# Kernel optimization log

Hardware: AMD Instinct MI355X
Metric: run time of the kernel (lower is better)

Reference implementation:

```python
import jax, jax.numpy as jnp
import numpy as np

T, X_D, M_N, CHUNK, REDUCE = 2048, 2048, 64, 64, 8
M_D = X_D // REDUCE          # 256
DECAY_D = M_D // 4           # 64
H_D = X_D * 2                # factor=2
FF_D = 256 * round(int(H_D * (2.0 / 3.0)) / 256)  # 2816


def setup_inputs() -> dict:
    key = jax.random.key(0)
    ks = jax.random.split(key, 20)
    def lin(k, out_d, in_d):
        return (jax.random.normal(k, (out_d, in_d), jnp.float32) / np.sqrt(in_d).astype(np.float32))
    return {
        "xs": jax.random.normal(ks[0], (T, X_D), jnp.float32),
        "attn_q": lin(ks[1], X_D // REDUCE, X_D),
        "attn_k": lin(ks[2], X_D // REDUCE, X_D // REDUCE),
        "attn_v": lin(ks[3], X_D, X_D),
        "attn_o": lin(ks[4], X_D, X_D),
        "attn_r": lin(ks[5], X_D, X_D),
        "mem_f": lin(ks[6], M_N, X_D),
        "mem_q": lin(ks[7], M_D, X_D),
        "mem_k": lin(ks[8], M_D, M_D),
        "mem_v": lin(ks[9], M_D, X_D),
        "mem_o": lin(ks[10], X_D, M_D),
        "mem_r": lin(ks[11], X_D, X_D),
        "mem_beta": -jnp.ones((M_N, M_D), jnp.float32),
        "mem_decay": 3.0 * jnp.ones((M_N, DECAY_D), jnp.float32),
        "mem_l": jax.random.uniform(ks[12], (M_N, M_D), dtype=jnp.float32),
        "ff_in1": lin(ks[13], FF_D, X_D),
        "ff_in2": lin(ks[14], FF_D, X_D),
        "ff_out": lin(ks[15], X_D, FF_D),
        "sn1_g": jnp.sqrt(jnp.float32(X_D)),
        "sn2_g": jnp.sqrt(jnp.float32(X_D)),
    }


def _rotate_half(x):
    x1 = x[..., ::2]
    x2 = x[..., 1::2]
    return jnp.stack((-x2, x1), axis=-1).reshape(x.shape)


def _scale_norm(x, g):
    return x * (g / (jnp.linalg.norm(x, axis=-1, keepdims=True) + 1e-8))


def _attn(xs, Wq, Wk, Wv, Wo, Wr):
    n = CHUNK
    q = xs @ Wq.T                       # (T, dk)
    k = q @ Wk.T                        # k is computed from q (as in source)
    v = xs @ Wv.T                       # (T, x_d)
    c = xs.shape[0] // n
    dk = q.shape[-1]
    q = q.reshape(c, n, dk)
    k = k.reshape(c, n, dk)
    v = v.reshape(c, n, v.shape[-1])

    def with_prev(a):                   # prepend previous chunk (zero for chunk 0)
        prev = jnp.concatenate([jnp.zeros_like(a[:1]), a[:-1]], axis=0)
        return jnp.concatenate([prev, a], axis=1)   # (c, 2n, d)

    k2, v2 = with_prev(k), with_prev(v)

    # RoPE over 2n key positions; queries take the last n positions
    inv_freq = 1.0 / (10000.0 ** (jnp.arange(0, dk, 2, dtype=jnp.float32) / dk))
    ang = jnp.arange(2 * n, dtype=jnp.float32)[:, None] * inv_freq[None, :]
    sin = jnp.repeat(jnp.sin(ang), 2, axis=-1)      # (2n, dk) interleaved
    cos = jnp.repeat(jnp.cos(ang), 2, axis=-1)
    q = q * cos[None, n:] + _rotate_half(q) * sin[None, n:]
    k2 = k2 * cos[None] + _rotate_half(k2) * sin[None]

    qk = jnp.einsum('cnk,cmk->cnm', q, k2) / jnp.sqrt(jnp.float32(dk))
    allowed = jnp.arange(2 * n)[None, :] <= (jnp.arange(n)[:, None] + n)  # tril offset n
    A = jax.nn.softmax(jnp.where(allowed[None], qk, -jnp.inf), axis=-1)
    y = jnp.einsum('cnm,cmv->cnv', A, v2).reshape(xs.shape[0], -1)
    return (y @ Wo.T) * jax.nn.sigmoid(xs @ Wr.T)


def _mem(xs, Wf, Wq, Wk, Wv, Wo, Wr, beta_p, decay_p, l_p):
    v = xs @ Wv.T                                       # (T, m_d)
    f = jax.nn.sigmoid(xs @ Wf.T)[:, :, None]           # (T, m_n, 1)
    beta = jax.nn.sigmoid(beta_p)[None]                 # (1, m_n, m_d)
    gamma = jnp.concatenate(
        [jnp.ones((M_N, M_D - DECAY_D), xs.dtype), jax.nn.sigmoid(decay_p)], axis=1
    )[None]                                             # (1, m_n, m_d)
    ws = (1.0 - f * beta) * gamma                       # (T, m_n, m_d)
    fvs = f * v[:, None, :]                             # (T, m_n, m_d)

    def bin_assoc(ei, ej):
        ai, bi = ei
        aj, bj = ej
        return (aj * ai, aj * bi + bj)

    _, mems = jax.lax.associative_scan(bin_assoc, (ws, fvs), axis=0)  # (T, m_n, m_d)

    q = xs @ Wq.T                                       # (T, m_d)
    k = jnp.einsum('nmd,kd->nmk', mems, Wk) + l_p[None]
    A = jax.nn.softmax(jnp.einsum('nmk,nk->nm', k, q) / jnp.sqrt(jnp.float32(M_D)), axis=-1)
    y = jnp.einsum('nm,nmd->nd', A, mems)
    return (y @ Wo.T) * jax.nn.sigmoid(xs @ Wr.T)


def _ff(xs, W1, W2, Wo):
    return (jax.nn.silu(xs @ W1.T) * (xs @ W2.T)) @ Wo.T


def reference(xs, attn_q, attn_k, attn_v, attn_o, attn_r,
              mem_f, mem_q, mem_k, mem_v, mem_o, mem_r,
              mem_beta, mem_decay, mem_l,
              ff_in1, ff_in2, ff_out, sn1_g, sn2_g):
    xn = _scale_norm(xs, sn1_g)
    xs = (_attn(xn, attn_q, attn_k, attn_v, attn_o, attn_r)
          + _mem(xn, mem_f, mem_q, mem_k, mem_v, mem_o, mem_r, mem_beta, mem_decay, mem_l)
          + xs)
    xs = _ff(_scale_norm(xs, sn2_g), ff_in1, ff_in2, ff_out) + xs
    return xs
```

## Files before the change

kernel.cpp:

```cpp
#include <hip/hip_runtime.h>
#include <math.h>


typedef short bhalf8 __attribute__((ext_vector_type(8)));
typedef float f32x4 __attribute__((ext_vector_type(4)));

#define CC_LD 7168
#define COL_V   0
#define COL_B1  2048
#define COL_B2  4096
#define COL_QB  6144
#define COL_VM  6400
#define COL_QM  6656
#define COL_FG  6912

#define AS1 __attribute__((address_space(1)))
#define AS3 __attribute__((address_space(3)))

__device__ __forceinline__ float sigmoidf_(float x){ return 1.0f/(1.0f+expf(-x)); }

__device__ __forceinline__ unsigned short f2b(float f){
  unsigned u = __float_as_uint(f);
  unsigned r = (u + 0x7fffu + ((u>>16)&1u)) >> 16;
  return (unsigned short)r;
}
__device__ __forceinline__ float b2f(unsigned short h){
  return __uint_as_float(((unsigned)h)<<16);
}

__global__ void k_f2b_all(
    const float* __restrict__ av, const float* __restrict__ ar, const float* __restrict__ mr,
    const float* __restrict__ aq, const float* __restrict__ mv, const float* __restrict__ mq,
    const float* __restrict__ mf, const float* __restrict__ ao, const float* __restrict__ mo,
    const float* __restrict__ f1, const float* __restrict__ f2, const float* __restrict__ fo,
    const float* __restrict__ ak,
    unsigned short* __restrict__ WCAT, unsigned short* __restrict__ AOB,
    unsigned short* __restrict__ MOB, unsigned short* __restrict__ FFW,
    unsigned short* __restrict__ FFOB, unsigned short* __restrict__ AKB){
  int i = blockIdx.x*256 + threadIdx.x;
  const float* s; unsigned short* d; int off;
  if (i < 3571712){
    d = WCAT + (size_t)i*4;
    if      (i < 1048576){ s = av; off = i; }
    else if (i < 2097152){ s = ar; off = i-1048576; }
    else if (i < 3145728){ s = mr; off = i-2097152; }
    else if (i < 3276800){ s = aq; off = i-3145728; }
    else if (i < 3407872){ s = mv; off = i-3276800; }
    else if (i < 3538944){ s = mq; off = i-3407872; }
    else                 { s = mf; off = i-3538944; }
  }
  else if (i < 4620288){ off = i-3571712; s = ao; d = AOB  + (size_t)off*4; }
  else if (i < 4751360){ off = i-4620288; s = mo; d = MOB  + (size_t)off*4; }
  else if (i < 6193152){ off = i-4751360; s = f1;
    int row = off >> 9, c4 = off & 511;
    d = FFW + ((size_t)row*2)*2048 + c4*4; }
  else if (i < 7634944){ off = i-6193152; s = f2;
    int row = off >> 9, c4 = off & 511;
    d = FFW + ((size_t)row*2 + 1)*2048 + c4*4; }
  else if (i < 9076736){ off = i-7634944; s = fo; d = FFOB + (size_t)off*4; }
  else if (i < 9093120){ off = i-9076736; s = ak; d = AKB  + (size_t)off*4; }
  else return;
  float4 v = ((const float4*)s)[off];
  ushort4 o;
  o.x = f2b(v.x); o.y = f2b(v.y); o.z = f2b(v.z); o.w = f2b(v.w);
  *(ushort4*)d = o;
}

__global__ void k_f2bT(const float* __restrict__ s, unsigned short* __restrict__ d){
  int i = blockIdx.x, j = threadIdx.x;
  d[(size_t)j*256 + i] = f2b(s[(size_t)i*256 + j]);
}

__global__ void k_trig(float2* __restrict__ TR){
  int idx = blockIdx.x*256 + threadIdx.x;
  int pos = idx >> 7, j = idx & 127;
  float inv = powf(10000.f, -(float)j/128.f);
  float a = (float)pos * inv;
  TR[idx] = make_float2(cosf(a), sinf(a));
}

__global__ __launch_bounds__(256) void k_scalenorm_b(const float* __restrict__ x,
    const float* __restrict__ g, unsigned short* __restrict__ ob){
  int row = blockIdx.x, tid = threadIdx.x;
  const float* xr = x + (size_t)row*2048;
  float ss = 0.f;
  for (int j = tid; j < 2048; j += 256){ float v = xr[j]; ss += v*v; }
  __shared__ float red[256];
  red[tid] = ss; __syncthreads();
  for (int s = 128; s > 0; s >>= 1){ if (tid < s) red[tid] += red[tid+s]; __syncthreads(); }
  float scale = g[0] / (sqrtf(red[0]) + 1e-8f);
  unsigned short* orow = ob + (size_t)row*2048;
  for (int j4 = tid; j4 < 512; j4 += 256){
    float4 v = *(const float4*)(xr + j4*4);
    ushort4 o;
    o.x = f2b(v.x*scale); o.y = f2b(v.y*scale); o.z = f2b(v.z*scale); o.w = f2b(v.w*scale);
    ((ushort4*)orow)[j4] = o;
  }
}

__global__ __launch_bounds__(256) void k_gemm_p(
    const unsigned short* __restrict__ A, int lda,
    const unsigned short* __restrict__ B,
    float* __restrict__ C, unsigned short* __restrict__ Cb,
    int N, int K, int ldc, int epi,
    const float* __restrict__ add,
    const unsigned short* __restrict__ gate, int gate_ld,
    const unsigned short* A2, const unsigned short* B2, float* C2){
  __shared__ unsigned short LDSu[24576];
  int tid = threadIdx.x;
  int w = tid >> 6, l = tid & 63;
  int bi = blockIdx.y, bj = blockIdx.x;
  const unsigned short* Ap = A; const unsigned short* Bp = B; float* Cp = C;
  if (blockIdx.z){ Ap = A2; Bp = B2; Cp = C2; }
  int m0 = bi*128, n0 = bj*128;
  int wr = w >> 1, wc = w & 1;

  f32x4 acc[4][4];
#pragma unroll
  for (int i=0;i<4;++i)
#pragma unroll
    for (int j=0;j<4;++j){ f32x4 z = {0.f,0.f,0.f,0.f}; acc[i][j] = z; }

  const int r0 = tid >> 2;
  const int gsrc8 = (((tid&3) ^ ((tid>>3)&3)) * 8);

  auto stage = [&](int bs, int kt){
    unsigned short* db = LDSu + bs*8192;
    const unsigned short* ap0 = Ap + (size_t)(m0 + r0)*lda      + kt*32 + gsrc8;
    const unsigned short* ap1 = Ap + (size_t)(m0 + 64 + r0)*lda + kt*32 + gsrc8;
    const unsigned short* bp0 = Bp + (size_t)(n0 + r0)*K        + kt*32 + gsrc8;
    const unsigned short* bp1 = Bp + (size_t)(n0 + 64 + r0)*K   + kt*32 + gsrc8;
    __builtin_amdgcn_global_load_lds((const AS1 void*)ap0, (AS3 void*)(db + tid*8),        16, 0, 0);
    __builtin_amdgcn_global_load_lds((const AS1 void*)ap1, (AS3 void*)(db + 2048 + tid*8), 16, 0, 0);
    __builtin_amdgcn_global_load_lds((const AS1 void*)bp0, (AS3 void*)(db + 4096 + tid*8), 16, 0, 0);
    __builtin_amdgcn_global_load_lds((const AS1 void*)bp1, (AS3 void*)(db + 6144 + tid*8), 16, 0, 0);
  };

  const int nt = K >> 5;
  stage(0, 0);
  stage(1, 1);
  asm volatile("s_waitcnt vmcnt(4)" ::: "memory");
  __builtin_amdgcn_s_barrier();

  const int lr = l & 15;
  const int gsw = (((l>>4) ^ ((l>>1)&3)) * 8);
  const int aoff = (wr*64 + lr)*32 + gsw;
  const int boff = 4096 + (wc*64 + lr)*32 + gsw;

  int cur = 0;
  for (int t = 0; t < nt; ++t){
    if (t + 2 < nt) stage((t+2)%3, t+2);
    const unsigned short* Tb = LDSu + cur*8192;
    bhalf8 af[4], bfr[4];
#pragma unroll
    for (int m=0;m<4;++m) af[m]  = *(const bhalf8*)(Tb + aoff + m*512);
#pragma unroll
    for (int n=0;n<4;++n) bfr[n] = *(const bhalf8*)(Tb + boff + n*512);
    __builtin_amdgcn_s_setprio(1);
#pragma unroll
    for (int m=0;m<4;++m)
#pragma unroll
      for (int n=0;n<4;++n)
        acc[m][n] = __builtin_amdgcn_mfma_f32_16x16x32_bf16(af[m], bfr[n], acc[m][n], 0, 0, 0);
    __builtin_amdgcn_s_setprio(0);
    if (t + 1 < nt){
      if (t + 2 < nt){ asm volatile("s_waitcnt vmcnt(4)" ::: "memory"); }
      else           { asm volatile("s_waitcnt vmcnt(0)" ::: "memory"); }
      __builtin_amdgcn_s_barrier();
      cur = (cur == 2) ? 0 : cur + 1;
    }
  }

#pragma unroll
  for (int m=0;m<4;++m){
    int rowb = m0 + wr*64 + m*16 + ((l>>4)<<2);
#pragma unroll
    for (int r=0;r<4;++r){
      int row = rowb + r;
      size_t rbase = (size_t)row*ldc;
      size_t gbase = (size_t)row*gate_ld;
#pragma unroll
      for (int n=0;n<4;++n){
        int col = n0 + wc*64 + n*16 + (l&15);
        float v = acc[m][n][r];
        if (epi == 4){
          float o = __shfl_xor(v, 1);
          if ((l & 1) == 0)
            Cb[gbase + (col>>1)] = f2b(v*sigmoidf_(v)*o);
          continue;
        }
        if (add) v += add[rbase + col];
        if (epi == 2) v *= sigmoidf_(b2f(gate[gbase + col]));
        if (epi == 3) Cb[rbase + col] = f2b(v);
        else          Cp[rbase + col] = v;
      }
    }
  }
}

__global__ __launch_bounds__(256) void k_gemm_fuse2(
    const unsigned short* __restrict__ A,  const unsigned short* __restrict__ B,
    const unsigned short* __restrict__ A2, const unsigned short* __restrict__ B2,
    const unsigned short* __restrict__ gate1, const unsigned short* __restrict__ gate2,
    const float* __restrict__ xs, float* __restrict__ XS2){
  __shared__ unsigned short LDSu[24576];
  int tid = threadIdx.x;
  int w = tid >> 6, l = tid & 63;
  int bi = blockIdx.y, bj = blockIdx.x;
  int m0 = bi*128, n0 = bj*128;
  int wr = w >> 1, wc = w & 1;

  f32x4 acc[4][4], acc2[4][4];
#pragma unroll
  for (int i=0;i<4;++i)
#pragma unroll
    for (int j=0;j<4;++j){ f32x4 z = {0.f,0.f,0.f,0.f}; acc[i][j] = z; acc2[i][j] = z; }

  const int r0 = tid >> 2;
  const int gsrc8 = (((tid&3) ^ ((tid>>3)&3)) * 8);

  auto stage = [&](int bs, int kt, const unsigned short* Ap, int lda,
                   const unsigned short* Bp, int ldb){
    unsigned short* db = LDSu + bs*8192;
    const unsigned short* ap0 = Ap + (size_t)(m0 + r0)*lda      + kt*32 + gsrc8;
    const unsigned short* ap1 = Ap + (size_t)(m0 + 64 + r0)*lda + kt*32 + gsrc8;
    const unsigned short* bp0 = Bp + (size_t)(n0 + r0)*ldb      + kt*32 + gsrc8;
    const unsigned short* bp1 = Bp + (size_t)(n0 + 64 + r0)*ldb + kt*32 + gsrc8;
    __builtin_amdgcn_global_load_lds((const AS1 void*)ap0, (AS3 void*)(db + tid*8),        16, 0, 0);
    __builtin_amdgcn_global_load_lds((const AS1 void*)ap1, (AS3 void*)(db + 2048 + tid*8), 16, 0, 0);
    __builtin_amdgcn_global_load_lds((const AS1 void*)bp0, (AS3 void*)(db + 4096 + tid*8), 16, 0, 0);
    __builtin_amdgcn_global_load_lds((const AS1 void*)bp1, (AS3 void*)(db + 6144 + tid*8), 16, 0, 0);
  };

  const int lr = l & 15;
  const int gsw = (((l>>4) ^ ((l>>1)&3)) * 8);
  const int aoff = (wr*64 + lr)*32 + gsw;
  const int boff = 4096 + (wc*64 + lr)*32 + gsw;

  {
    const int nt = 64;
    stage(0, 0, A, 2048, B, 2048);
    stage(1, 1, A, 2048, B, 2048);
    asm volatile("s_waitcnt vmcnt(4)" ::: "memory");
    __builtin_amdgcn_s_barrier();
    int cur = 0;
    for (int t = 0; t < nt; ++t){
      if (t + 2 < nt) stage((t+2)%3, t+2, A, 2048, B, 2048);
      const unsigned short* Tb = LDSu + cur*8192;
      bhalf8 af[4], bfr[4];
#pragma unroll
      for (int m=0;m<4;++m) af[m]  = *(const bhalf8*)(Tb + aoff + m*512);
#pragma unroll
      for (int n=0;n<4;++n) bfr[n] = *(const bhalf8*)(Tb + boff + n*512);
      __builtin_amdgcn_s_setprio(1);
#pragma unroll
      for (int m=0;m<4;++m)
#pragma unroll
        for (int n=0;n<4;++n)
          acc[m][n] = __builtin_amdgcn_mfma_f32_16x16x32_bf16(af[m], bfr[n], acc[m][n], 0, 0, 0);
      __builtin_amdgcn_s_setprio(0);
      if (t + 1 < nt){
        if (t + 2 < nt){ asm volatile("s_waitcnt vmcnt(4)" ::: "memory"); }
        else           { asm volatile("s_waitcnt vmcnt(0)" ::: "memory"); }
        __builtin_amdgcn_s_barrier();
        cur = (cur == 2) ? 0 : cur + 1;
      }
    }
  }
  __syncthreads();

  {
    const int nt = 8;
    stage(0, 0, A2, 256, B2, 256);
    stage(1, 1, A2, 256, B2, 256);
    asm volatile("s_waitcnt vmcnt(4)" ::: "memory");
    __builtin_amdgcn_s_barrier();
    int cur = 0;
    for (int t = 0; t < nt; ++t){
      if (t + 2 < nt) stage((t+2)%3, t+2, A2, 256, B2, 256);
      const unsigned short* Tb = LDSu + cur*8192;
      bhalf8 af[4], bfr[4];
#pragma unroll
      for (int m=0;m<4;++m) af[m]  = *(const bhalf8*)(Tb + aoff + m*512);
#pragma unroll
      for (int n=0;n<4;++n) bfr[n] = *(const bhalf8*)(Tb + boff + n*512);
      __builtin_amdgcn_s_setprio(1);
#pragma unroll
      for (int m=0;m<4;++m)
#pragma unroll
        for (int n=0;n<4;++n)
          acc2[m][n] = __builtin_amdgcn_mfma_f32_16x16x32_bf16(af[m], bfr[n], acc2[m][n], 0, 0, 0);
      __builtin_amdgcn_s_setprio(0);
      if (t + 1 < nt){
        if (t + 2 < nt){ asm volatile("s_waitcnt vmcnt(4)" ::: "memory"); }
        else           { asm volatile("s_waitcnt vmcnt(0)" ::: "memory"); }
        __builtin_amdgcn_s_barrier();
        cur = (cur == 2) ? 0 : cur + 1;
      }
    }
  }

#pragma unroll
  for (int m=0;m<4;++m){
    int rowb = m0 + wr*64 + m*16 + ((l>>4)<<2);
#pragma unroll
    for (int r=0;r<4;++r){
      int row = rowb + r;
      size_t gb = (size_t)row*CC_LD;
      size_t rb = (size_t)row*2048;
#pragma unroll
      for (int n=0;n<4;++n){
        int col = n0 + wc*64 + n*16 + (l&15);
        float v = acc[m][n][r]*sigmoidf_(b2f(gate1[gb + col]))
                + acc2[m][n][r]*sigmoidf_(b2f(gate2[gb + col]))
                + xs[rb + col];
        XS2[rb + col] = v;
      }
    }
  }
}

__global__ __launch_bounds__(256) void k_attn_scores_mfma(
    const unsigned short* __restrict__ CCqb, const float* __restrict__ K0,
    const float2* __restrict__ TR, unsigned short* __restrict__ P){
  __shared__ unsigned short Ks[128*256];
  int c = blockIdx.x, tid = threadIdx.x;
  for (int it = 0; it < 16; ++it){
    int id = tid + it*256;
    int m = id >> 5;
    int cs = (id & 31) * 8;
    float v[8];
    if (c == 0 && m < 64){
#pragma unroll
      for (int u=0;u<8;++u) v[u] = 0.f;
    } else {
      int gr = (c-1)*64 + m;
      const float* kr = K0 + (size_t)gr*256 + cs;
      float4 x0 = *(const float4*)kr, x1 = *(const float4*)(kr+4);
      v[0]=x0.x; v[1]=x0.y; v[2]=x0.z; v[3]=x0.w;
      v[4]=x1.x; v[5]=x1.y; v[6]=x1.z; v[7]=x1.w;
#pragma unroll
      for (int p2=0;p2<4;++p2){
        float2 t = TR[m*128 + (cs>>1) + p2];
        float e = v[2*p2], o = v[2*p2+1];
        v[2*p2]   = e*t.x - o*t.y;
        v[2*p2+1] = o*t.x + e*t.y;
      }
    }
    unsigned short pk[8];
#pragma unroll
    for (int u=0;u<8;++u) pk[u] = f2b(v[u]);
    int byte = m*512 + ((cs*2) ^ ((m&7)<<4));
    *(bhalf8*)((char*)&Ks[0] + byte) = *(const bhalf8*)pk;
  }
  __syncthreads();

  int w = tid >> 6, l = tid & 63;
  int lr = l & 15, lkg = l >> 4;
  f32x4 acc[8];
#pragma unroll
  for (int n=0;n<8;++n){ f32x4 z = {0.f,0.f,0.f,0.f}; acc[n] = z; }

  int iq = w*16 + lr;
  const unsigned short* qbase = CCqb + (size_t)(c*64 + iq)*CC_LD;
  int pos = 64 + iq;

  for (int kt = 0; kt < 8; ++kt){
    int k0c = kt*32 + lkg*8;
    bhalf8 q8 = *(const bhalf8*)(qbase + k0c);
    float v[8];
#pragma unroll
    for (int u=0;u<8;++u) v[u] = b2f((unsigned short)(((short*)&q8)[u]));
#pragma unroll
    for (int p2=0;p2<4;++p2){
      float2 t = TR[pos*128 + (k0c>>1) + p2];
      float e = v[2*p2], o = v[2*p2+1];
      v[2*p2]   = e*t.x - o*t.y;
      v[2*p2+1] = o*t.x + e*t.y;
    }
    unsigned short pk[8];
#pragma unroll
    for (int u=0;u<8;++u) pk[u] = f2b(v[u]);
    bhalf8 af = *(const bhalf8*)pk;
#pragma unroll
    for (int n=0;n<8;++n){
      int m = n*16 + lr;
      int byte = m*512 + ((k0c*2) ^ ((m&7)<<4));
      bhalf8 bf = *(const bhalf8*)((const char*)&Ks[0] + byte);
      acc[n] = __builtin_amdgcn_mfma_f32_16x16x32_bf16(af, bf, acc[n], 0, 0, 0);
    }
  }

  int i0 = w*16 + lkg*4;
  float mx[4] = {-1e30f,-1e30f,-1e30f,-1e30f};
  float sm[4] = {0.f,0.f,0.f,0.f};
#pragma unroll
  for (int n=0;n<8;++n){
    int col = n*16 + lr;
#pragma unroll
    for (int r=0;r<4;++r){
      float vv = acc[n][r] * (1.f/16.f);
      if (col > i0 + r + 64) vv = -1e30f;
      acc[n][r] = vv;
      mx[r] = fmaxf(mx[r], vv);
    }
  }
#pragma unroll
  for (int s=1; s<16; s<<=1)
#pragma unroll
    for (int r=0;r<4;++r) mx[r] = fmaxf(mx[r], __shfl_xor(mx[r], s));
#pragma unroll
  for (int n=0;n<8;++n)
#pragma unroll
    for (int r=0;r<4;++r){
      float e = expf(acc[n][r] - mx[r]);
      acc[n][r] = e; sm[r] += e;
    }
#pragma unroll
  for (int s=1; s<16; s<<=1)
#pragma unroll
    for (int r=0;r<4;++r) sm[r] += __shfl_xor(sm[r], s);
  float rcp[4];
#pragma unroll
  for (int r=0;r<4;++r) rcp[r] = 1.f/sm[r];

  unsigned short* Pr = P + (size_t)c*8192;
#pragma unroll
  for (int n=0;n<8;++n){
    int col = n*16 + lr;
#pragma unroll
    for (int r=0;r<4;++r)
      Pr[(i0+r)*128 + col] = f2b(acc[n][r]*rcp[r]);
  }
}

__global__ __launch_bounds__(256) void k_attn_pv_mfma(
    const unsigned short* __restrict__ P, const unsigned short* __restrict__ Vb, int vld,
    unsigned short* __restrict__ Y){
  __shared__ unsigned short Vt[128*128];
  int ct = blockIdx.x, c = blockIdx.y, tid = threadIdx.x;
  {
    int k = tid >> 1;
    int ch = (tid & 1) * 64;
    if (c == 0 && k < 64){
      for (int u=0; u<64; ++u){
        int col = ch + u;
        int byte = col*256 + ((k*2) ^ ((col&7)<<4));
        *(unsigned short*)((char*)&Vt[0] + byte) = 0;
      }
    } else {
      int gr = (c-1)*64 + k;
      const unsigned short* vr = Vb + (size_t)gr*vld + ct*128 + ch;
      for (int u8=0; u8<8; ++u8){
        bhalf8 x = *(const bhalf8*)(vr + u8*8);
#pragma unroll
        for (int u=0;u<8;++u){
          int col = ch + u8*8 + u;
          int byte = col*256 + ((k*2) ^ ((col&7)<<4));
          *(unsigned short*)((char*)&Vt[0] + byte) = (unsigned short)(((short*)&x)[u]);
        }
      }
    }
  }
  __syncthreads();
  int w = tid >> 6, l = tid & 63, lr = l & 15, lkg = l >> 4;
  f32x4 acc[8];
#pragma unroll
  for (int n=0;n<8;++n){ f32x4 z = {0.f,0.f,0.f,0.f}; acc[n] = z; }
  const unsigned short* Pr = P + (size_t)c*8192;
  for (int kt=0; kt<4; ++kt){
    int kb = kt*32 + lkg*8;
    bhalf8 af = *(const bhalf8*)(Pr + (w*16 + lr)*128 + kb);
#pragma unroll
    for (int n=0;n<8;++n){
      int col = n*16 + lr;
      int byte = col*256 + ((kb*2) ^ ((col&7)<<4));
      bhalf8 bf = *(const bhalf8*)((const char*)&Vt[0] + byte);
      acc[n] = __builtin_amdgcn_mfma_f32_16x16x32_bf16(af, bf, acc[n], 0, 0, 0);
    }
  }
  int row0 = c*64 + w*16 + lkg*4;
#pragma unroll
  for (int n=0;n<8;++n){
    int col = ct*128 + n*16 + lr;
#pragma unroll
    for (int r=0;r<4;++r)
      Y[(size_t)(row0+r)*2048 + col] = f2b(acc[n][r]);
  }
}

__global__ __launch_bounds__(256) void k_scan1(const unsigned short* __restrict__ CC,
    const float* __restrict__ beta_p, const float* __restrict__ decay_p,
    float* __restrict__ CP, float* __restrict__ CQ){
  int c = blockIdx.x, mg = blockIdx.y, d = threadIdx.x;
  __shared__ float Fs[512];
  for (int v = threadIdx.x; v < 512; v += 256){
    int s = v >> 3, j = v & 7;
    Fs[v] = sigmoidf_(b2f(CC[(size_t)(c*64+s)*CC_LD + COL_FG + mg*8 + j]));
  }
  __syncthreads();
  float beta[8], gamma[8], Pa[8], Qa[8];
#pragma unroll
  for (int j=0;j<8;++j){
    int m = mg*8+j;
    beta[j]  = sigmoidf_(beta_p[m*256+d]);
    gamma[j] = (d < 192) ? 1.f : sigmoidf_(decay_p[m*64 + (d-192)]);
    Pa[j] = 1.f; Qa[j] = 0.f;
  }
  for (int s = 0; s < 64; ++s){
    float vm = b2f(CC[(size_t)(c*64+s)*CC_LD + COL_VM + d]);
#pragma unroll
    for (int j=0;j<8;++j){
      float f = Fs[s*8+j];
      float w = (1.f - f*beta[j])*gamma[j];
      Pa[j] *= w;
      Qa[j] = w*Qa[j] + f*vm;
    }
  }
#pragma unroll
  for (int j=0;j<8;++j){
    size_t idx = ((size_t)c*64 + mg*8 + j)*256 + d;
    CP[idx] = Pa[j]; CQ[idx] = Qa[j];
  }
}

__global__ __launch_bounds__(256) void k_scan2(const float* __restrict__ CP,
    const float* __restrict__ CQ, float* __restrict__ SIN){
  int m = blockIdx.x, d = threadIdx.x;
  float S = 0.f;
  for (int c = 0; c < 32; ++c){
    size_t idx = ((size_t)c*64 + m)*256 + d;
    SIN[idx] = S;
    S = CP[idx]*S + CQ[idx];
  }
}

__global__ __launch_bounds__(256) void k_scan3(const unsigned short* __restrict__ CC,
    const float* __restrict__ beta_p, const float* __restrict__ decay_p,
    const float* __restrict__ SIN, unsigned short* __restrict__ MEMS){
  int c = blockIdx.x, mg = blockIdx.y, d = threadIdx.x;
  __shared__ float Fs[512];
  for (int v = threadIdx.x; v < 512; v += 256){
    int s = v >> 3, j = v & 7;
    Fs[v] = sigmoidf_(b2f(CC[(size_t)(c*64+s)*CC_LD + COL_FG + mg*8 + j]));
  }
  __syncthreads();
  float beta[8], gamma[8], S[8];
#pragma unroll
  for (int j=0;j<8;++j){
    int m = mg*8+j;
    beta[j]  = sigmoidf_(beta_p[m*256+d]);
    gamma[j] = (d < 192) ? 1.f : sigmoidf_(decay_p[m*64 + (d-192)]);
    S[j] = SIN[((size_t)c*64 + m)*256 + d];
  }
  for (int s = 0; s < 64; ++s){
    float vm = b2f(CC[(size_t)(c*64+s)*CC_LD + COL_VM + d]);
    size_t tb = (size_t)(c*64+s)*64;
#pragma unroll
    for (int j=0;j<8;++j){
      float f = Fs[s*8+j];
      float w = (1.f - f*beta[j])*gamma[j];
      S[j] = w*S[j] + f*vm;
      MEMS[(tb + mg*8 + j)*256 + d] = f2b(S[j]);
    }
  }
}

__global__ __launch_bounds__(256) void k_memread(const unsigned short* __restrict__ MEMS,
    const float* __restrict__ QH, const unsigned short* __restrict__ QMs, int qm_ld,
    const float* __restrict__ L, unsigned short* __restrict__ YMb){
  int t = blockIdx.x, tid = threadIdx.x;
  int wave = tid >> 6, lane = tid & 63;
  __shared__ float anorm[64];
  const unsigned short* Mt = MEMS + (size_t)t*16384;
  float4 qh4 = *(const float4*)(QH + (size_t)t*256 + lane*4);
  ushort4 qmu = *(const ushort4*)(QMs + (size_t)t*qm_ld + lane*4);
  float qm0 = b2f(qmu.x), qm1 = b2f(qmu.y), qm2 = b2f(qmu.z), qm3 = b2f(qmu.w);
  for (int mi = 0; mi < 16; ++mi){
    int m = wave*16 + mi;
    ushort4 su = *(const ushort4*)(Mt + m*256 + lane*4);
    float4 l4 = *(const float4*)(L + (size_t)m*256 + lane*4);
    float p = b2f(su.x)*qh4.x + b2f(su.y)*qh4.y + b2f(su.z)*qh4.z + b2f(su.w)*qh4.w
            + l4.x*qm0 + l4.y*qm1 + l4.z*qm2 + l4.w*qm3;
#pragma unroll
    for (int off = 32; off > 0; off >>= 1) p += __shfl_down(p, off);
    if (lane == 0) anorm[m] = p * (1.f/16.f);
  }
  __syncthreads();
  if (tid < 64){
    float v = anorm[tid];
    float mx = v;
#pragma unroll
    for (int off = 32; off > 0; off >>= 1) mx = fmaxf(mx, __shfl_xor(mx, off));
    float e = expf(v - mx);
    float s = e;
#pragma unroll
    for (int off = 32; off > 0; off >>= 1) s += __shfl_xor(s, off);
    anorm[tid] = e / s;
  }
  __syncthreads();
  float acc = 0.f;
  for (int m = 0; m < 64; ++m) acc += anorm[m]*b2f(Mt[m*256 + tid]);
  YMb[(size_t)t*256 + tid] = f2b(acc);
}

extern "C" void kernel_launch(void* const* d_in, const int* in_sizes, int n_in,
                              void* d_out, int out_size, void* d_ws, size_t ws_size,
                              hipStream_t stream){
  const float* xs        = (const float*)d_in[0];
  const float* attn_q    = (const float*)d_in[1];
  const float* attn_k    = (const float*)d_in[2];
  const float* attn_v    = (const float*)d_in[3];
  const float* attn_o    = (const float*)d_in[4];
  const float* attn_r    = (const float*)d_in[5];
  const float* mem_f     = (const float*)d_in[6];
  const float* mem_q     = (const float*)d_in[7];
  const float* mem_k     = (const float*)d_in[8];
  const float* mem_v     = (const float*)d_in[9];
  const float* mem_o     = (const float*)d_in[10];
  const float* mem_r     = (const float*)d_in[11];
  const float* mem_beta  = (const float*)d_in[12];
  const float* mem_decay = (const float*)d_in[13];
  const float* mem_l     = (const float*)d_in[14];
  const float* ff1       = (const float*)d_in[15];
  const float* ff2       = (const float*)d_in[16];
  const float* ffo       = (const float*)d_in[17];
  const float* sn1       = (const float*)d_in[18];
  const float* sn2       = (const float*)d_in[19];
  float* out = (float*)d_out;
  float* W = (float*)d_ws;

  unsigned short* XNb  = (unsigned short*)(W + 0);
  unsigned short* WCAT = (unsigned short*)(W + 2097152);
  unsigned short* CCb  = (unsigned short*)(W + 9437184);
  unsigned short* AOB  = (unsigned short*)(W + 16777216);
  unsigned short* MOB  = (unsigned short*)(W + 18874368);
  unsigned short* FFW  = (unsigned short*)(W + 19136512);
  unsigned short* FFOB = (unsigned short*)(W + 24903680);
  unsigned short* AKB  = (unsigned short*)(W + 27787264);
  unsigned short* MKTB = (unsigned short*)(W + 27820032);
  unsigned short* Ybb  = (unsigned short*)(W + 27852800);
  float*          XS2  = W + 34144256;
  unsigned short* MEMSb= (unsigned short*)(W + 38338560);
  float*          CP   = W + 55115776;
  float*          CQ   = W + 55640064;
  float*          SIN  = W + 56164352;
  float2*         TRIG = (float2*)(W + 0);
  float*          K0   = W + 32768;
  unsigned short* P    = (unsigned short*)(W + 557056);
  float*          QH   = W + 688128;
  unsigned short* YMb  = (unsigned short*)(W + 1212416);
  unsigned short* XN2b = MEMSb;
  unsigned short* H1b  = (unsigned short*)(W + 40435712);

  dim3 blk(256);

  k_f2b_all<<<dim3(35520), blk, 0, stream>>>(attn_v, attn_r, mem_r, attn_q, mem_v, mem_q,
      mem_f, attn_o, mem_o, ff1, ff2, ffo, attn_k, WCAT, AOB, MOB, FFW, FFOB, AKB);
  k_f2bT<<<dim3(256), blk, 0, stream>>>(mem_k, MKTB);

  k_scalenorm_b<<<dim3(2048), blk, 0, stream>>>(xs, sn1, XNb);

  k_gemm_p<<<dim3(56, 16), blk, 0, stream>>>(XNb, 2048, WCAT, nullptr, CCb, CC_LD, 2048, CC_LD, 3,
      nullptr, nullptr, 0, nullptr, nullptr, nullptr);

  k_trig<<<dim3(64), blk, 0, stream>>>(TRIG);

  k_gemm_p<<<dim3(2, 16, 2), blk, 0, stream>>>(CCb + COL_QB, CC_LD, AKB, K0, nullptr, 256, 256, 256, 0,
      nullptr, nullptr, 0, CCb + COL_QM, MKTB, QH);

  k_attn_scores_mfma<<<dim3(32), blk, 0, stream>>>(CCb + COL_QB, K0, TRIG, P);
  k_attn_pv_mfma<<<dim3(16, 32), blk, 0, stream>>>(P, CCb + COL_V, CC_LD, Ybb);

  k_scan1<<<dim3(32, 8), blk, 0, stream>>>(CCb, mem_beta, mem_decay, CP, CQ);
  k_scan2<<<dim3(64), blk, 0, stream>>>(CP, CQ, SIN);
  k_scan3<<<dim3(32, 8), blk, 0, stream>>>(CCb, mem_beta, mem_decay, SIN, MEMSb);
  k_memread<<<dim3(2048), blk, 0, stream>>>(MEMSb, QH, CCb + COL_QM, CC_LD, mem_l, YMb);

  k_gemm_fuse2<<<dim3(16, 16), blk, 0, stream>>>(Ybb, AOB, YMb, MOB,
      CCb + COL_B1, CCb + COL_B2, xs, XS2);

  k_scalenorm_b<<<dim3(2048), blk, 0, stream>>>(XS2, sn2, XN2b);

  k_gemm_p<<<dim3(44, 16), blk, 0, stream>>>(XN2b, 2048, FFW, nullptr, H1b, 5632, 2048, 5632, 4,
      nullptr, nullptr, 2816, nullptr, nullptr, nullptr);
  k_gemm_p<<<dim3(16, 16), blk, 0, stream>>>(H1b, 2816, FFOB, out, nullptr, 2048, 2816, 2048, 0,
      XS2, nullptr, 0, nullptr, nullptr, nullptr);
}
```

Before: 416.5 us.

## Use 256x256-tile 512-thread GEMM kernel for the two largest projections

Adds a new GEMM kernel with 256x256 output tiles, 8 waves per block and a triple-buffered LDS pipeline of 96 KB. It replaces the 128x128 GEMM for the fused input projection (N=7168) and the FF up-projection with the SiLU-gate epilogue. Larger tiles raise arithmetic intensity and cut global reloads of A and B. The trade-off is fewer blocks (224 and 176 on a 256-CU part), which risks under-filling the GPU and lowering occupancy because of the larger LDS and register use.

Result: no change. 421.6 us (+1.2%).

```diff
diff --git a/kernel.cpp b/kernel.cpp
--- a/kernel.cpp
+++ b/kernel.cpp
@@ -98,6 +98,97 @@
   }
 }
 
+__global__ __launch_bounds__(512) void k_gemm_big(
+    const unsigned short* __restrict__ A, int lda,
+    const unsigned short* __restrict__ B,
+    unsigned short* __restrict__ Cb, int K, int ldc, int epi, int gate_ld){
+  __shared__ unsigned short LDSu[49152];
+  int tid = threadIdx.x;
+  int w = tid >> 6, l = tid & 63;
+  int bi = blockIdx.y, bj = blockIdx.x;
+  int m0 = bi*256, n0 = bj*256;
+  int wr = w >> 2, wc = w & 3;
+
+  f32x4 acc[8][4];
+#pragma unroll
+  for (int i=0;i<8;++i)
+#pragma unroll
+    for (int j=0;j<4;++j){ f32x4 z = {0.f,0.f,0.f,0.f}; acc[i][j] = z; }
+
+  const int r0 = tid >> 2;
+  const int gsrc8 = (((tid&3) ^ ((tid>>3)&3)) * 8);
+
+  auto stage = [&](int bs, int kt){
+    unsigned short* db = LDSu + bs*16384;
+    const unsigned short* ap0 = A + (size_t)(m0 + r0)*lda       + kt*32 + gsrc8;
+    const unsigned short* ap1 = A + (size_t)(m0 + 128 + r0)*lda + kt*32 + gsrc8;
+    const unsigned short* bp0 = B + (size_t)(n0 + r0)*K         + kt*32 + gsrc8;
+    const unsigned short* bp1 = B + (size_t)(n0 + 128 + r0)*K   + kt*32 + gsrc8;
+    __builtin_amdgcn_global_load_lds((const AS1 void*)ap0, (AS3 void*)(db + tid*8),         16, 0, 0);
+    __builtin_amdgcn_global_load_lds((const AS1 void*)ap1, (AS3 void*)(db + 4096 + tid*8),  16, 0, 0);
+    __builtin_amdgcn_global_load_lds((const AS1 void*)bp0, (AS3 void*)(db + 8192 + tid*8),  16, 0, 0);
+    __builtin_amdgcn_global_load_lds((const AS1 void*)bp1, (AS3 void*)(db + 12288 + tid*8), 16, 0, 0);
+  };
+
+  const int nt = K >> 5;
+  stage(0, 0);
+  stage(1, 1);
+  asm volatile("s_waitcnt vmcnt(4)" ::: "memory");
+  __builtin_amdgcn_s_barrier();
+
+  const int lr = l & 15;
+  const int gsw = (((l>>4) ^ ((l>>1)&3)) * 8);
+  const int aoff = (wr*128 + lr)*32 + gsw;
+  const int boff = 8192 + (wc*64 + lr)*32 + gsw;
+
+  int cur = 0;
+  for (int t = 0; t < nt; ++t){
+    if (t + 2 < nt) stage((t+2)%3, t+2);
+    const unsigned short* Tb = LDSu + cur*16384;
+    bhalf8 bfr[4];
+#pragma unroll
+    for (int n=0;n<4;++n) bfr[n] = *(const bhalf8*)(Tb + boff + n*512);
+    __builtin_amdgcn_s_setprio(1);
+#pragma unroll
+    for (int fr=0;fr<8;++fr){
+      bhalf8 af = *(const bhalf8*)(Tb + aoff + fr*512);
+#pragma unroll
+      for (int n=0;n<4;++n)
+        acc[fr][n] = __builtin_amdgcn_mfma_f32_16x16x32_bf16(af, bfr[n], acc[fr][n], 0, 0, 0);
+    }
+    __builtin_amdgcn_s_setprio(0);
+    if (t + 1 < nt){
+      if (t + 2 < nt){ asm volatile("s_waitcnt vmcnt(4)" ::: "memory"); }
+      else           { asm volatile("s_waitcnt vmcnt(0)" ::: "memory"); }
+      __builtin_amdgcn_s_barrier();
+      cur = (cur == 2) ? 0 : cur + 1;
+    }
+  }
+
+#pragma unroll
+  for (int fr=0;fr<8;++fr){
+    int rowb = m0 + wr*128 + fr*16 + ((l>>4)<<2);
+#pragma unroll
+    for (int r=0;r<4;++r){
+      int row = rowb + r;
+      size_t rbase = (size_t)row*ldc;
+      size_t gbase = (size_t)row*gate_ld;
+#pragma unroll
+      for (int n=0;n<4;++n){
+        int col = n0 + wc*64 + n*16 + (l&15);
+        float v = acc[fr][n][r];
+        if (epi == 4){
+          float o = __shfl_xor(v, 1);
+          if ((l & 1) == 0)
+            Cb[gbase + (col>>1)] = f2b(v*sigmoidf_(v)*o);
+        } else {
+          Cb[rbase + col] = f2b(v);
+        }
+      }
+    }
+  }
+}
+
 __global__ __launch_bounds__(256) void k_gemm_p(
     const unsigned short* __restrict__ A, int lda,
     const unsigned short* __restrict__ B,
@@ -183,12 +274,6 @@
       for (int n=0;n<4;++n){
         int col = n0 + wc*64 + n*16 + (l&15);
         float v = acc[m][n][r];
-        if (epi == 4){
-          float o = __shfl_xor(v, 1);
-          if ((l & 1) == 0)
-            Cb[gbase + (col>>1)] = f2b(v*sigmoidf_(v)*o);
-          continue;
-        }
         if (add) v += add[rbase + col];
         if (epi == 2) v *= sigmoidf_(b2f(gate[gbase + col]));
         if (epi == 3) Cb[rbase + col] = f2b(v);
@@ -654,6 +739,7 @@
   unsigned short* H1b  = (unsigned short*)(W + 40435712);
 
   dim3 blk(256);
+  dim3 blk512(512);
 
   k_f2b_all<<<dim3(35520), blk, 0, stream>>>(attn_v, attn_r, mem_r, attn_q, mem_v, mem_q,
       mem_f, attn_o, mem_o, ff1, ff2, ffo, attn_k, WCAT, AOB, MOB, FFW, FFOB, AKB);
@@ -661,8 +747,7 @@
 
   k_scalenorm_b<<<dim3(2048), blk, 0, stream>>>(xs, sn1, XNb);
 
-  k_gemm_p<<<dim3(56, 16), blk, 0, stream>>>(XNb, 2048, WCAT, nullptr, CCb, CC_LD, 2048, CC_LD, 3,
-      nullptr, nullptr, 0, nullptr, nullptr, nullptr);
+  k_gemm_big<<<dim3(28, 8), blk512, 0, stream>>>(XNb, 2048, WCAT, CCb, 2048, CC_LD, 3, 0);
 
   k_trig<<<dim3(64), blk, 0, stream>>>(TRIG);
 
@@ -682,8 +767,7 @@
 
   k_scalenorm_b<<<dim3(2048), blk, 0, stream>>>(XS2, sn2, XN2b);
 
-  k_gemm_p<<<dim3(44, 16), blk, 0, stream>>>(XN2b, 2048, FFW, nullptr, H1b, 5632, 2048, 5632, 4,
-      nullptr, nullptr, 2816, nullptr, nullptr, nullptr);
+  k_gemm_big<<<dim3(22, 8), blk512, 0, stream>>>(XN2b, 2048, FFW, H1b, 2048, 5632, 4, 2816);
   k_gemm_p<<<dim3(16, 16), blk, 0, stream>>>(H1b, 2816, FFOB, out, nullptr, 2048, 2816, 2048, 0,
       XS2, nullptr, 0, nullptr, nullptr, nullptr);
 }
```
